# Optimization experiments

Measured on AMD Instinct MI355X. Metric: run time of the kernel, lower is better.

The kernel has to match this reference:

```python
import jax, jax.numpy as jnp
import numpy as np

N = 8192
NFEAT = 512
NHID = 512
NCLASS = 64
NLAYERS = 8
LAMDA = 0.5
ALPHA = 0.1
EDGE_P = 0.002  # ~16 avg degree


def setup_inputs() -> dict:
    key = jax.random.key(0)
    ks = jax.random.split(key, 6)
    x = jax.random.normal(ks[0], (N, NFEAT), dtype=jnp.float32)
    # sparse 0/1 adjacency, densified (the original densifies adj each layer)
    adj = (jax.random.uniform(ks[1], (N, N)) < EDGE_P).astype(jnp.float32)
    stdv1 = 1.0 / np.sqrt(NHID)
    fc1_W = jax.random.normal(ks[2], (NFEAT, NHID), dtype=jnp.float32) * stdv1
    fc1_b = jnp.zeros((NHID,), dtype=jnp.float32)
    # GraphConvolution.reset_parameters: uniform(-1/sqrt(out), 1/sqrt(out))
    conv_Ws = jax.random.uniform(ks[3], (NLAYERS, NHID, NHID), minval=-stdv1, maxval=stdv1, dtype=jnp.float32)
    stdv2 = 1.0 / np.sqrt(NCLASS)
    fc2_W = jax.random.normal(ks[4], (NHID, NCLASS), dtype=jnp.float32) * stdv2
    fc2_b = jnp.zeros((NCLASS,), dtype=jnp.float32)
    return {"x": x, "adj": adj, "fc1_W": fc1_W, "fc1_b": fc1_b,
            "conv_Ws": conv_Ws, "fc2_W": fc2_W, "fc2_b": fc2_b}


def reference(x, adj, fc1_W, fc1_b, conv_Ws, fc2_W, fc2_b):
    n = adj.shape[0]
    # A_hat = A + I ; P = D^{-1/2} A_hat D^{-1/2}  (diag matmuls -> row/col scaling)
    A_hat = adj + jnp.eye(n, dtype=adj.dtype)
    dinv = 1.0 / jnp.sqrt(jnp.sum(A_hat, axis=0))  # [N]
    P = dinv[:, None] * A_hat * dinv[None, :]      # identical every layer; compute once

    H0 = jax.nn.relu(x @ fc1_W + fc1_b)            # fc1 (dropout is identity: training=False)
    H = H0
    for i in range(NLAYERS):
        beta = float(np.log(LAMDA / (i + 1) + 1.0))
        init_res = (1.0 - ALPHA) * (P @ H) + ALPHA * H0
        # init_res @ ((1-beta) I + beta W) expanded:
        H = jax.nn.relu((1.0 - beta) * init_res + beta * (init_res @ conv_Ws[i]))
    logits = H @ fc2_W + fc2_b
    return -jax.nn.log_softmax(logits, axis=1)
```

## Files before the change

kernel.cpp:

```cpp
#include <hip/hip_runtime.h>
#include <hip/hip_bf16.h>
#include <cmath>

#define N_NODES 8192
#define NFEAT 512
#define NHID 512
#define NCLASS 64
#define NLAYERS 8
#define CAP 96

typedef __attribute__((ext_vector_type(8))) short bf16x8;
typedef __attribute__((ext_vector_type(4))) float f32x4;
typedef unsigned short u16;

__device__ inline float bf2f(short u) {
  union { unsigned int i; float f; } x;
  x.i = ((unsigned int)(u16)u) << 16;
  return x.f;
}
__device__ inline short f2bf(float f) {
  union { float f; unsigned int i; } x;
  x.f = f;
  unsigned int r = x.i + 0x7FFFu + ((x.i >> 16) & 1u);
  return (short)(r >> 16);
}

__global__ __launch_bounds__(256)
void extract_kernel(const float* __restrict__ adj, int* __restrict__ idx,
                    int* __restrict__ cnt, int* __restrict__ colcnt)
{
  __shared__ int s_cnt;
  const int i = blockIdx.x;
  if (threadIdx.x == 0) s_cnt = 0;
  __syncthreads();
  const uint4* row = (const uint4*)(adj + (size_t)i * N_NODES);
  for (int c = threadIdx.x; c < N_NODES / 4; c += 256) {
    uint4 v = row[c];
    if ((v.x | v.y | v.z | v.w) == 0u) continue;
    unsigned int vals[4] = {v.x, v.y, v.z, v.w};
    #pragma unroll
    for (int e = 0; e < 4; ++e) {
      if (vals[e] != 0u) {
        int p = atomicAdd(&s_cnt, 1);
        if (p < CAP) idx[(size_t)i * CAP + p] = c * 4 + e;
        atomicAdd(&colcnt[c * 4 + e], 1);
      }
    }
  }
  __syncthreads();
  if (threadIdx.x == 0) cnt[i] = min(s_cnt, CAP);
}

__global__ __launch_bounds__(256)
void dinv_kernel(const int* __restrict__ colcnt, float* __restrict__ dinv)
{
  int j = blockIdx.x * 256 + threadIdx.x;
  if (j < N_NODES) dinv[j] = 1.0f / sqrtf((float)colcnt[j] + 1.0f);
}

__global__ __launch_bounds__(256)
void cvt_bf16_kernel(const float* __restrict__ src, u16* __restrict__ dst, int n4)
{
  int i = blockIdx.x * 256 + threadIdx.x;
  if (i >= n4) return;
  float4 v = ((const float4*)src)[i];
  ushort4 o;
  o.x = (u16)f2bf(v.x); o.y = (u16)f2bf(v.y);
  o.z = (u16)f2bf(v.z); o.w = (u16)f2bf(v.w);
  ((ushort4*)dst)[i] = o;
}

struct Coefs { float cA[8]; float cB[8]; };

__global__ __launch_bounds__(256)
void transpose_cast_kernel(const float* __restrict__ fc1W, const float* __restrict__ convW,
                           const float* __restrict__ fc2W,
                           u16* __restrict__ Wt, u16* __restrict__ Wt2, Coefs co)
{
  __shared__ float tile[32][33];
  const int m = blockIdx.z;
  const int k0 = blockIdx.x * 32, n0 = blockIdx.y * 32;
  if (m == 9 && n0 >= 64) return;
  const int tx = threadIdx.x & 31, ty = threadIdx.x >> 5;
  if (m == 9) {
    #pragma unroll
    for (int r = 0; r < 32; r += 8)
      tile[ty + r][tx] = fc2W[(size_t)(k0 + ty + r) * 64 + n0 + tx];
    __syncthreads();
    #pragma unroll
    for (int r = 0; r < 32; r += 8)
      Wt2[(size_t)(n0 + ty + r) * 512 + k0 + tx] = (u16)f2bf(tile[tx][ty + r]);
    return;
  }
  const float* src = (m == 0) ? fc1W : convW + (size_t)(m - 1) * NHID * NHID;
  u16* dst = Wt + (size_t)m * NHID * NHID;
  float cA = 0.f, cB = 1.f;
  if (m >= 1) { cA = co.cA[m - 1]; cB = co.cB[m - 1]; }
  #pragma unroll
  for (int r = 0; r < 32; r += 8)
    tile[ty + r][tx] = src[(size_t)(k0 + ty + r) * NHID + n0 + tx];
  __syncthreads();
  #pragma unroll
  for (int r = 0; r < 32; r += 8) {
    const int krow = k0 + tx, ncol = n0 + ty + r;
    float val = cB * tile[tx][ty + r];
    if (m >= 1 && krow == ncol) val += cA;
    dst[(size_t)ncol * NHID + krow] = (u16)f2bf(val);
  }
}

#define AS1 __attribute__((address_space(1)))
#define AS3 __attribute__((address_space(3)))

__device__ inline void load16(const void* g, void* l) {
  __builtin_amdgcn_global_load_lds((const AS1 void*)g, (AS3 void*)l, 16, 0, 0);
}

template<int MODE>
__global__ __launch_bounds__(256, 4)
void gemm_kernel(const u16* __restrict__ A, const u16* __restrict__ Bt,
                 const float* __restrict__ bias, const float* __restrict__ dinv,
                 u16* __restrict__ out0, u16* __restrict__ out1,
                 float* __restrict__ outF)
{
  constexpr int K = 512;
  constexpr int N = (MODE == 3) ? NCLASS : 512;
  __shared__ u16 lds[2][2][64 * 64];
  const int tid = threadIdx.x;
  const int wave = tid >> 6, lane = tid & 63;

  const int cpx = gridDim.x >> 3;
  const int logical = (blockIdx.x & 7) * cpx + (blockIdx.x >> 3);
  const int mblk = (MODE == 3) ? logical : (logical >> 3);
  const int nblk = (MODE == 3) ? 0 : (logical & 7);
  const int m0 = mblk * 64, n0 = nblk * 64;

  const int wr = wave >> 1, wc = wave & 1;
  const int lrow = lane & 15, lk = lane >> 4;

  f32x4 acc[2][2];
  #pragma unroll
  for (int a = 0; a < 2; ++a)
    #pragma unroll
    for (int b = 0; b < 2; ++b)
      acc[a][b] = (f32x4){0.f, 0.f, 0.f, 0.f};

  auto stage = [&](int b, int ks) {
    #pragma unroll
    for (int r = 0; r < 2; ++r) {
      const int c = r * 256 + wave * 64 + lane;
      const int row = c >> 3;
      const int sc = (c & 7) ^ (row & 7);
      load16(A  + (size_t)(m0 + row) * K + ks + sc * 8, &lds[b][0][(r * 256 + wave * 64) * 8]);
      load16(Bt + (size_t)(n0 + row) * K + ks + sc * 8, &lds[b][1][(r * 256 + wave * 64) * 8]);
    }
  };

  stage(0, 0);
  __syncthreads();

  for (int t = 0; t < 8; ++t) {
    const int b = t & 1;
    if (t + 1 < 8) stage(b ^ 1, (t + 1) * 64);
    const char* pA = (const char*)lds[b][0];
    const char* pB = (const char*)lds[b][1];
    bf16x8 af[2][2], bfr[2][2];
    #pragma unroll
    for (int mi = 0; mi < 2; ++mi) {
      const int row = wr * 32 + mi * 16 + lrow;
      #pragma unroll
      for (int ks2 = 0; ks2 < 2; ++ks2) {
        const int j = ks2 * 4 + lk;
        af[mi][ks2] = *(const bf16x8*)(pA + row * 128 + ((j ^ (row & 7)) * 16));
      }
    }
    #pragma unroll
    for (int ni = 0; ni < 2; ++ni) {
      const int row = wc * 32 + ni * 16 + lrow;
      #pragma unroll
      for (int ks2 = 0; ks2 < 2; ++ks2) {
        const int j = ks2 * 4 + lk;
        bfr[ni][ks2] = *(const bf16x8*)(pB + row * 128 + ((j ^ (row & 7)) * 16));
      }
    }
    #pragma unroll
    for (int ks2 = 0; ks2 < 2; ++ks2)
      #pragma unroll
      for (int mi = 0; mi < 2; ++mi)
        #pragma unroll
        for (int ni = 0; ni < 2; ++ni)
          acc[mi][ni] = __builtin_amdgcn_mfma_f32_16x16x32_bf16(af[mi][ks2], bfr[ni][ks2], acc[mi][ni], 0, 0, 0);
    __syncthreads();
  }

  if (MODE != 3) {
    #pragma unroll
    for (int mi = 0; mi < 2; ++mi) {
      #pragma unroll
      for (int ni = 0; ni < 2; ++ni) {
        #pragma unroll
        for (int r = 0; r < 4; ++r) {
          const int row = m0 + wr * 32 + mi * 16 + lk * 4 + r;
          const int col = n0 + wc * 32 + ni * 16 + lrow;
          const size_t o = (size_t)row * N + col;
          float v = acc[mi][ni][r];
          if (MODE == 0) {
            v = fmaxf(v + bias[col], 0.f);
            out0[o] = (u16)f2bf(v);
            out1[o] = (u16)f2bf(dinv[row] * v);
          } else {
            v = fmaxf(v, 0.f);
            out0[o] = (u16)f2bf(MODE == 1 ? dinv[row] * v : v);
          }
        }
      }
    }
  } else {
    float* Cf = (float*)&lds[0][0][0];
    #pragma unroll
    for (int mi = 0; mi < 2; ++mi)
      #pragma unroll
      for (int ni = 0; ni < 2; ++ni)
        #pragma unroll
        for (int r = 0; r < 4; ++r) {
          const int row = wr * 32 + mi * 16 + lk * 4 + r;
          const int col = wc * 32 + ni * 16 + lrow;
          Cf[row * 65 + col] = acc[mi][ni][r] + bias[col];
        }
    __syncthreads();
    #pragma unroll 4
    for (int r = 0; r < 16; ++r) {
      const int row = wave * 16 + r;
      const float v = Cf[row * 65 + lane];
      float mx = v;
      #pragma unroll
      for (int off = 32; off > 0; off >>= 1) mx = fmaxf(mx, __shfl_xor(mx, off));
      float s = __expf(v - mx);
      #pragma unroll
      for (int off = 32; off > 0; off >>= 1) s += __shfl_xor(s, off);
      outF[(size_t)(m0 + row) * NCLASS + lane] = -(v - mx - logf(s));
    }
  }
}

__global__ __launch_bounds__(256)
void spmm_kernel(const u16* __restrict__ Hs, const u16* __restrict__ H0,
                 const float* __restrict__ dinv, const int* __restrict__ idx,
                 const int* __restrict__ cnt, u16* __restrict__ IR)
{
  const int wave = threadIdx.x >> 6, lane = threadIdx.x & 63;
  const int i = blockIdx.x * 4 + wave;
  const int c0 = lane * 8;
  const int n = cnt[i];
  int jreg = 0;
  if (lane < n) jreg = idx[(size_t)i * CAP + lane] & (N_NODES - 1);

  float acc[8];
  #pragma unroll
  for (int e = 0; e < 8; ++e) acc[e] = 0.f;

  const int nn = min(n, 64);
  int t = 0;
  for (; t + 8 <= nn; t += 8) {
    bf16x8 v[8];
    #pragma unroll
    for (int u = 0; u < 8; ++u) {
      const int j = __shfl(jreg, t + u);
      v[u] = *(const bf16x8*)&Hs[(size_t)j * NHID + c0];
    }
    #pragma unroll
    for (int u = 0; u < 8; ++u)
      #pragma unroll
      for (int e = 0; e < 8; ++e)
        acc[e] += bf2f(v[u][e]);
  }
  for (; t < nn; ++t) {
    const int j = __shfl(jreg, t);
    bf16x8 v = *(const bf16x8*)&Hs[(size_t)j * NHID + c0];
    #pragma unroll
    for (int e = 0; e < 8; ++e) acc[e] += bf2f(v[e]);
  }
  for (; t < n; ++t) {
    const int j = idx[(size_t)i * CAP + t] & (N_NODES - 1);
    bf16x8 v = *(const bf16x8*)&Hs[(size_t)j * NHID + c0];
    #pragma unroll
    for (int e = 0; e < 8; ++e) acc[e] += bf2f(v[e]);
  }

  const float di = dinv[i];
  bf16x8 self = *(const bf16x8*)&Hs[(size_t)i * NHID + c0];
  bf16x8 h0   = *(const bf16x8*)&H0[(size_t)i * NHID + c0];
  bf16x8 ov;
  #pragma unroll
  for (int e = 0; e < 8; ++e) {
    float v = 0.9f * di * (acc[e] + bf2f(self[e])) + 0.1f * bf2f(h0[e]);
    ov[e] = f2bf(v);
  }
  *(bf16x8*)&IR[(size_t)i * NHID + c0] = ov;
}

extern "C" void kernel_launch(void* const* d_in, const int* in_sizes, int n_in,
                              void* d_out, int out_size, void* d_ws, size_t ws_size,
                              hipStream_t stream)
{
  const float* x     = (const float*)d_in[0];
  const float* adj   = (const float*)d_in[1];
  const float* fc1W  = (const float*)d_in[2];
  const float* fc1b  = (const float*)d_in[3];
  const float* convW = (const float*)d_in[4];
  const float* fc2W  = (const float*)d_in[5];
  const float* fc2b  = (const float*)d_in[6];
  float* out = (float*)d_out;

  char* ws = (char*)d_ws;
  size_t off = 0;
  auto alloc = [&](size_t bytes) -> void* {
    void* p = ws + off;
    off = (off + bytes + 255) & ~(size_t)255;
    return p;
  };
  u16*   xb   = (u16*)alloc((size_t)N_NODES * NFEAT * 2);
  u16*   Wt   = (u16*)alloc((size_t)9 * NHID * NHID * 2);
  u16*   Wt2  = (u16*)alloc((size_t)NCLASS * NHID * 2);
  u16*   H0   = (u16*)alloc((size_t)N_NODES * NHID * 2);
  u16*   HsA  = (u16*)alloc((size_t)N_NODES * NHID * 2);
  u16*   HsB  = (u16*)alloc((size_t)N_NODES * NHID * 2);
  u16*   IR   = (u16*)alloc((size_t)N_NODES * NHID * 2);
  int*   idx  = (int*)alloc((size_t)N_NODES * CAP * 4);
  int*   cnt  = (int*)alloc((size_t)N_NODES * 4);
  int*   colc = (int*)alloc((size_t)N_NODES * 4);
  float* dinv = (float*)alloc((size_t)N_NODES * 4);

  Coefs co;
  for (int i = 0; i < NLAYERS; ++i) {
    const double beta = log(0.5 / (double)(i + 1) + 1.0);
    co.cA[i] = (float)(1.0 - beta);
    co.cB[i] = (float)beta;
  }

  hipMemsetAsync(colc, 0, N_NODES * 4, stream);
  extract_kernel<<<N_NODES, 256, 0, stream>>>(adj, idx, cnt, colc);
  dinv_kernel<<<N_NODES / 256, 256, 0, stream>>>(colc, dinv);
  cvt_bf16_kernel<<<(N_NODES * NFEAT / 4) / 256, 256, 0, stream>>>(x, xb, N_NODES * NFEAT / 4);
  transpose_cast_kernel<<<dim3(16, 16, 10), 256, 0, stream>>>(fc1W, convW, fc2W, Wt, Wt2, co);

  gemm_kernel<0><<<1024, 256, 0, stream>>>(xb, Wt, fc1b, dinv, H0, HsA, nullptr);

  const u16* Hin = HsA;
  for (int i = 0; i < NLAYERS; ++i) {
    spmm_kernel<<<N_NODES / 4, 256, 0, stream>>>(Hin, H0, dinv, idx, cnt, IR);
    u16* Hout = (Hin == HsA) ? HsB : HsA;
    if (i < NLAYERS - 1)
      gemm_kernel<1><<<1024, 256, 0, stream>>>(
          IR, Wt + (size_t)(i + 1) * NHID * NHID, nullptr, dinv, Hout, nullptr, nullptr);
    else
      gemm_kernel<2><<<1024, 256, 0, stream>>>(
          IR, Wt + (size_t)(i + 1) * NHID * NHID, nullptr, dinv, Hout, nullptr, nullptr);
    Hin = Hout;
  }

  gemm_kernel<3><<<128, 256, 0, stream>>>((const u16*)Hin, Wt2, fc2b, nullptr, nullptr, nullptr, out);
}
```

Before: 305.3 us.

## Replace LDS-tiled dense GEMMs with register-resident-B GEMM and remap SpMM blocks

Adds a new GEMM kernel for the fc1 and per-layer conv projections. Each wave keeps a 16-column slice of the transposed weight in registers and streams A rows directly from global memory, with no LDS staging or barriers. The old kernel is reduced to a dedicated fc2 plus log-softmax kernel. The SpMM block index is also remapped so consecutive blocks land on different XCD-interleaved row groups. The trade-off is more global and L2 reads of A (each row is read by 32 column blocks) and more register use, in exchange for removing sync overhead.

```diff
diff --git a/kernel.cpp b/kernel.cpp
--- a/kernel.cpp
+++ b/kernel.cpp
@@ -109,6 +109,56 @@
   }
 }
 
+template<int MODE>
+__global__ __launch_bounds__(256, 4)
+void rgemm_kernel(const u16* __restrict__ A, const u16* __restrict__ Bt,
+                  const float* __restrict__ bias, const float* __restrict__ dinv,
+                  u16* __restrict__ out0, u16* __restrict__ out1)
+{
+  constexpr int K = 512, N = 512;
+  const int wave = threadIdx.x >> 6, lane = threadIdx.x & 63;
+  const int lrow = lane & 15, lk = lane >> 4;
+  const int mw = blockIdx.x * 256 + wave * 64;
+  const int n0 = blockIdx.y * 16;
+  const int col = n0 + lrow;
+
+  bf16x8 breg[16];
+  const u16* Brow = Bt + (size_t)col * K + lk * 8;
+  #pragma unroll
+  for (int ks = 0; ks < 16; ++ks)
+    breg[ks] = *(const bf16x8*)(Brow + ks * 32);
+
+  const float bb = (MODE == 0) ? bias[col] : 0.f;
+
+  #pragma unroll
+  for (int mt = 0; mt < 4; ++mt) {
+    const u16* Arow = A + (size_t)(mw + mt * 16 + lrow) * K + lk * 8;
+    f32x4 acc0 = (f32x4){0.f, 0.f, 0.f, 0.f};
+    f32x4 acc1 = (f32x4){0.f, 0.f, 0.f, 0.f};
+    #pragma unroll
+    for (int ks = 0; ks < 16; ks += 2) {
+      bf16x8 a0 = *(const bf16x8*)(Arow + ks * 32);
+      bf16x8 a1 = *(const bf16x8*)(Arow + ks * 32 + 32);
+      acc0 = __builtin_amdgcn_mfma_f32_16x16x32_bf16(a0, breg[ks],     acc0, 0, 0, 0);
+      acc1 = __builtin_amdgcn_mfma_f32_16x16x32_bf16(a1, breg[ks + 1], acc1, 0, 0, 0);
+    }
+    #pragma unroll
+    for (int r = 0; r < 4; ++r) {
+      const int row = mw + mt * 16 + lk * 4 + r;
+      const size_t o = (size_t)row * N + col;
+      float v = acc0[r] + acc1[r];
+      if (MODE == 0) {
+        v = fmaxf(v + bb, 0.f);
+        out0[o] = (u16)f2bf(v);
+        out1[o] = (u16)f2bf(dinv[row] * v);
+      } else {
+        v = fmaxf(v, 0.f);
+        out0[o] = (u16)f2bf(MODE == 1 ? dinv[row] * v : v);
+      }
+    }
+  }
+}
+
 #define AS1 __attribute__((address_space(1)))
 #define AS3 __attribute__((address_space(3)))
 
@@ -116,25 +166,17 @@
   __builtin_amdgcn_global_load_lds((const AS1 void*)g, (AS3 void*)l, 16, 0, 0);
 }
 
-template<int MODE>
 __global__ __launch_bounds__(256, 4)
-void gemm_kernel(const u16* __restrict__ A, const u16* __restrict__ Bt,
-                 const float* __restrict__ bias, const float* __restrict__ dinv,
-                 u16* __restrict__ out0, u16* __restrict__ out1,
-                 float* __restrict__ outF)
+void fc2_kernel(const u16* __restrict__ A, const u16* __restrict__ Bt,
+                const float* __restrict__ bias, float* __restrict__ outF)
 {
   constexpr int K = 512;
-  constexpr int N = (MODE == 3) ? NCLASS : 512;
   __shared__ u16 lds[2][2][64 * 64];
   const int tid = threadIdx.x;
   const int wave = tid >> 6, lane = tid & 63;
-
   const int cpx = gridDim.x >> 3;
   const int logical = (blockIdx.x & 7) * cpx + (blockIdx.x >> 3);
-  const int mblk = (MODE == 3) ? logical : (logical >> 3);
-  const int nblk = (MODE == 3) ? 0 : (logical & 7);
-  const int m0 = mblk * 64, n0 = nblk * 64;
-
+  const int m0 = logical * 64, n0 = 0;
   const int wr = wave >> 1, wc = wave & 1;
   const int lrow = lane & 15, lk = lane >> 4;
 
@@ -193,53 +235,29 @@
     __syncthreads();
   }
 
-  if (MODE != 3) {
-    #pragma unroll
-    for (int mi = 0; mi < 2; ++mi) {
-      #pragma unroll
-      for (int ni = 0; ni < 2; ++ni) {
-        #pragma unroll
-        for (int r = 0; r < 4; ++r) {
-          const int row = m0 + wr * 32 + mi * 16 + lk * 4 + r;
-          const int col = n0 + wc * 32 + ni * 16 + lrow;
-          const size_t o = (size_t)row * N + col;
-          float v = acc[mi][ni][r];
-          if (MODE == 0) {
-            v = fmaxf(v + bias[col], 0.f);
-            out0[o] = (u16)f2bf(v);
-            out1[o] = (u16)f2bf(dinv[row] * v);
-          } else {
-            v = fmaxf(v, 0.f);
-            out0[o] = (u16)f2bf(MODE == 1 ? dinv[row] * v : v);
-          }
-        }
-      }
-    }
-  } else {
-    float* Cf = (float*)&lds[0][0][0];
-    #pragma unroll
-    for (int mi = 0; mi < 2; ++mi)
-      #pragma unroll
-      for (int ni = 0; ni < 2; ++ni)
-        #pragma unroll
-        for (int r = 0; r < 4; ++r) {
-          const int row = wr * 32 + mi * 16 + lk * 4 + r;
-          const int col = wc * 32 + ni * 16 + lrow;
-          Cf[row * 65 + col] = acc[mi][ni][r] + bias[col];
-        }
-    __syncthreads();
-    #pragma unroll 4
-    for (int r = 0; r < 16; ++r) {
-      const int row = wave * 16 + r;
-      const float v = Cf[row * 65 + lane];
-      float mx = v;
-      #pragma unroll
-      for (int off = 32; off > 0; off >>= 1) mx = fmaxf(mx, __shfl_xor(mx, off));
-      float s = __expf(v - mx);
-      #pragma unroll
-      for (int off = 32; off > 0; off >>= 1) s += __shfl_xor(s, off);
-      outF[(size_t)(m0 + row) * NCLASS + lane] = -(v - mx - logf(s));
-    }
+  float* Cf = (float*)&lds[0][0][0];
+  #pragma unroll
+  for (int mi = 0; mi < 2; ++mi)
+    #pragma unroll
+    for (int ni = 0; ni < 2; ++ni)
+      #pragma unroll
+      for (int r = 0; r < 4; ++r) {
+        const int row = wr * 32 + mi * 16 + lk * 4 + r;
+        const int cc = wc * 32 + ni * 16 + lrow;
+        if (cc < NCLASS) Cf[row * 65 + cc] = acc[mi][ni][r] + bias[cc];
+      }
+  __syncthreads();
+  #pragma unroll 4
+  for (int r = 0; r < 16; ++r) {
+    const int row = wave * 16 + r;
+    const float v = Cf[row * 65 + lane];
+    float mx = v;
+    #pragma unroll
+    for (int off = 32; off > 0; off >>= 1) mx = fmaxf(mx, __shfl_xor(mx, off));
+    float s = __expf(v - mx);
+    #pragma unroll
+    for (int off = 32; off > 0; off >>= 1) s += __shfl_xor(s, off);
+    outF[(size_t)(m0 + row) * NCLASS + lane] = -(v - mx - logf(s));
   }
 }
 
@@ -249,7 +267,10 @@
                  const int* __restrict__ cnt, u16* __restrict__ IR)
 {
   const int wave = threadIdx.x >> 6, lane = threadIdx.x & 63;
-  const int i = blockIdx.x * 4 + wave;
+  const int b = blockIdx.x;
+  const int c = (b & 7) + 8 * ((b >> 3) >> 6);
+  const int j64 = (b >> 3) & 63;
+  const int i = (c * 64 + j64) * 4 + wave;
   const int c0 = lane * 8;
   const int n = cnt[i];
   int jreg = 0;
@@ -344,20 +365,20 @@
   cvt_bf16_kernel<<<(N_NODES * NFEAT / 4) / 256, 256, 0, stream>>>(x, xb, N_NODES * NFEAT / 4);
   transpose_cast_kernel<<<dim3(16, 16, 10), 256, 0, stream>>>(fc1W, convW, fc2W, Wt, Wt2, co);
 
-  gemm_kernel<0><<<1024, 256, 0, stream>>>(xb, Wt, fc1b, dinv, H0, HsA, nullptr);
+  rgemm_kernel<0><<<dim3(32, 32), 256, 0, stream>>>(xb, Wt, fc1b, dinv, H0, HsA);
 
   const u16* Hin = HsA;
   for (int i = 0; i < NLAYERS; ++i) {
     spmm_kernel<<<N_NODES / 4, 256, 0, stream>>>(Hin, H0, dinv, idx, cnt, IR);
     u16* Hout = (Hin == HsA) ? HsB : HsA;
     if (i < NLAYERS - 1)
-      gemm_kernel<1><<<1024, 256, 0, stream>>>(
-          IR, Wt + (size_t)(i + 1) * NHID * NHID, nullptr, dinv, Hout, nullptr, nullptr);
+      rgemm_kernel<1><<<dim3(32, 32), 256, 0, stream>>>(
+          IR, Wt + (size_t)(i + 1) * NHID * NHID, nullptr, dinv, Hout, nullptr);
     else
-      gemm_kernel<2><<<1024, 256, 0, stream>>>(
-          IR, Wt + (size_t)(i + 1) * NHID * NHID, nullptr, dinv, Hout, nullptr, nullptr);
+      rgemm_kernel<2><<<dim3(32, 32), 256, 0, stream>>>(
+          IR, Wt + (size_t)(i + 1) * NHID * NHID, nullptr, dinv, Hout, nullptr);
     Hin = Hout;
   }
 
-  gemm_kernel<3><<<128, 256, 0, stream>>>((const u16*)Hin, Wt2, fc2b, nullptr, nullptr, nullptr, out);
-}
+  fc2_kernel<<<128, 256, 0, stream>>>((const u16*)Hin, Wt2, fc2b, out);
+}
```

New measurement: 568.0 us. 1.86x slower.

## Merge preprocessing kernels, triple-buffer GEMM loads, compute dinv inline

Applied to the files above, without the earlier changes.

Extraction, input bf16 cast and weight transpose/cast now run as one front kernel with block-range dispatch, and the separate dinv kernel is dropped in favour of computing rsqrt(colcnt+1) inline where it is used. The GEMM goes from double to triple LDS buffering, with manual vmcnt waits plus a barrier so loads run two stages ahead, and its occupancy hint is lowered to 3. This cuts kernel launches and deepens load/compute overlap, at the cost of more LDS per block and possibly lower occupancy.

```diff
diff --git a/kernel.cpp b/kernel.cpp
--- a/kernel.cpp
+++ b/kernel.cpp
@@ -13,6 +13,8 @@
 typedef __attribute__((ext_vector_type(4))) float f32x4;
 typedef unsigned short u16;
 
+struct Coefs { float cA[8]; float cB[8]; };
+
 __device__ inline float bf2f(short u) {
   union { unsigned int i; float f; } x;
   x.i = ((unsigned int)(u16)u) << 16;
@@ -26,60 +28,59 @@
 }
 
 __global__ __launch_bounds__(256)
-void extract_kernel(const float* __restrict__ adj, int* __restrict__ idx,
-                    int* __restrict__ cnt, int* __restrict__ colcnt)
+void front_kernel(const float* __restrict__ adj, int* __restrict__ idx,
+                  int* __restrict__ cnt, int* __restrict__ colcnt,
+                  const float* __restrict__ x, u16* __restrict__ xb,
+                  const float* __restrict__ fc1W, const float* __restrict__ convW,
+                  const float* __restrict__ fc2W,
+                  u16* __restrict__ Wt, u16* __restrict__ Wt2, Coefs co)
 {
-  __shared__ int s_cnt;
-  const int i = blockIdx.x;
-  if (threadIdx.x == 0) s_cnt = 0;
-  __syncthreads();
-  const uint4* row = (const uint4*)(adj + (size_t)i * N_NODES);
-  for (int c = threadIdx.x; c < N_NODES / 4; c += 256) {
-    uint4 v = row[c];
-    if ((v.x | v.y | v.z | v.w) == 0u) continue;
-    unsigned int vals[4] = {v.x, v.y, v.z, v.w};
-    #pragma unroll
-    for (int e = 0; e < 4; ++e) {
-      if (vals[e] != 0u) {
-        int p = atomicAdd(&s_cnt, 1);
-        if (p < CAP) idx[(size_t)i * CAP + p] = c * 4 + e;
-        atomicAdd(&colcnt[c * 4 + e], 1);
+  __shared__ char smraw[4224];
+  const int bid = blockIdx.x;
+
+  if (bid < 8192) {
+    int* s_cnt = (int*)smraw;
+    const int i = bid;
+    if (threadIdx.x == 0) *s_cnt = 0;
+    __syncthreads();
+    const uint4* row = (const uint4*)(adj + (size_t)i * N_NODES);
+    for (int c = threadIdx.x; c < N_NODES / 4; c += 256) {
+      uint4 v = row[c];
+      if ((v.x | v.y | v.z | v.w) == 0u) continue;
+      unsigned int vals[4] = {v.x, v.y, v.z, v.w};
+      #pragma unroll
+      for (int e = 0; e < 4; ++e) {
+        if (vals[e] != 0u) {
+          int p = atomicAdd(s_cnt, 1);
+          if (p < CAP) idx[(size_t)i * CAP + p] = c * 4 + e;
+          atomicAdd(&colcnt[c * 4 + e], 1);
+        }
       }
     }
-  }
-  __syncthreads();
-  if (threadIdx.x == 0) cnt[i] = min(s_cnt, CAP);
-}
-
-__global__ __launch_bounds__(256)
-void dinv_kernel(const int* __restrict__ colcnt, float* __restrict__ dinv)
-{
-  int j = blockIdx.x * 256 + threadIdx.x;
-  if (j < N_NODES) dinv[j] = 1.0f / sqrtf((float)colcnt[j] + 1.0f);
-}
-
-__global__ __launch_bounds__(256)
-void cvt_bf16_kernel(const float* __restrict__ src, u16* __restrict__ dst, int n4)
-{
-  int i = blockIdx.x * 256 + threadIdx.x;
-  if (i >= n4) return;
-  float4 v = ((const float4*)src)[i];
-  ushort4 o;
-  o.x = (u16)f2bf(v.x); o.y = (u16)f2bf(v.y);
-  o.z = (u16)f2bf(v.z); o.w = (u16)f2bf(v.w);
-  ((ushort4*)dst)[i] = o;
-}
-
-struct Coefs { float cA[8]; float cB[8]; };
-
-__global__ __launch_bounds__(256)
-void transpose_cast_kernel(const float* __restrict__ fc1W, const float* __restrict__ convW,
-                           const float* __restrict__ fc2W,
-                           u16* __restrict__ Wt, u16* __restrict__ Wt2, Coefs co)
-{
-  __shared__ float tile[32][33];
-  const int m = blockIdx.z;
-  const int k0 = blockIdx.x * 32, n0 = blockIdx.y * 32;
+    __syncthreads();
+    if (threadIdx.x == 0) cnt[i] = min(*s_cnt, CAP);
+    return;
+  }
+
+  if (bid < 9216) {
+    const int base = (bid - 8192) * 256 + threadIdx.x;
+    const float4* src = (const float4*)x;
+    #pragma unroll
+    for (int it = 0; it < 4; ++it) {
+      const int i = it * (1024 * 256) + base;
+      float4 v = src[i];
+      ushort4 o;
+      o.x = (u16)f2bf(v.x); o.y = (u16)f2bf(v.y);
+      o.z = (u16)f2bf(v.z); o.w = (u16)f2bf(v.w);
+      ((ushort4*)xb)[i] = o;
+    }
+    return;
+  }
+
+  float (*tile)[33] = (float(*)[33])smraw;
+  const int vb = bid - 9216;
+  const int m = vb >> 8;
+  const int k0 = (vb & 15) * 32, n0 = ((vb >> 4) & 15) * 32;
   if (m == 9 && n0 >= 64) return;
   const int tx = threadIdx.x & 31, ty = threadIdx.x >> 5;
   if (m == 9) {
@@ -117,15 +118,15 @@
 }
 
 template<int MODE>
-__global__ __launch_bounds__(256, 4)
+__global__ __launch_bounds__(256, 3)
 void gemm_kernel(const u16* __restrict__ A, const u16* __restrict__ Bt,
-                 const float* __restrict__ bias, const float* __restrict__ dinv,
+                 const float* __restrict__ bias, const int* __restrict__ colc,
                  u16* __restrict__ out0, u16* __restrict__ out1,
                  float* __restrict__ outF)
 {
   constexpr int K = 512;
   constexpr int N = (MODE == 3) ? NCLASS : 512;
-  __shared__ u16 lds[2][2][64 * 64];
+  __shared__ u16 lds[3][2][64 * 64];
   const int tid = threadIdx.x;
   const int wave = tid >> 6, lane = tid & 63;
 
@@ -157,11 +158,13 @@
   };
 
   stage(0, 0);
-  __syncthreads();
+  stage(1, 64);
 
   for (int t = 0; t < 8; ++t) {
-    const int b = t & 1;
-    if (t + 1 < 8) stage(b ^ 1, (t + 1) * 64);
+    if (t < 7) asm volatile("s_waitcnt vmcnt(4)\n\ts_barrier" ::: "memory");
+    else       asm volatile("s_waitcnt vmcnt(0)\n\ts_barrier" ::: "memory");
+    if (t + 2 < 8) stage((t + 2) % 3, (t + 2) * 64);
+    const int b = t % 3;
     const char* pA = (const char*)lds[b][0];
     const char* pB = (const char*)lds[b][1];
     bf16x8 af[2][2], bfr[2][2];
@@ -190,7 +193,6 @@
         #pragma unroll
         for (int ni = 0; ni < 2; ++ni)
           acc[mi][ni] = __builtin_amdgcn_mfma_f32_16x16x32_bf16(af[mi][ks2], bfr[ni][ks2], acc[mi][ni], 0, 0, 0);
-    __syncthreads();
   }
 
   if (MODE != 3) {
@@ -206,16 +208,22 @@
           float v = acc[mi][ni][r];
           if (MODE == 0) {
             v = fmaxf(v + bias[col], 0.f);
+            const float di = rsqrtf((float)colc[row] + 1.0f);
             out0[o] = (u16)f2bf(v);
-            out1[o] = (u16)f2bf(dinv[row] * v);
+            out1[o] = (u16)f2bf(di * v);
+          } else if (MODE == 1) {
+            v = fmaxf(v, 0.f);
+            const float di = rsqrtf((float)colc[row] + 1.0f);
+            out0[o] = (u16)f2bf(di * v);
           } else {
             v = fmaxf(v, 0.f);
-            out0[o] = (u16)f2bf(MODE == 1 ? dinv[row] * v : v);
+            out0[o] = (u16)f2bf(v);
           }
         }
       }
     }
   } else {
+    __syncthreads();
     float* Cf = (float*)&lds[0][0][0];
     #pragma unroll
     for (int mi = 0; mi < 2; ++mi)
@@ -224,8 +232,8 @@
         #pragma unroll
         for (int r = 0; r < 4; ++r) {
           const int row = wr * 32 + mi * 16 + lk * 4 + r;
-          const int col = wc * 32 + ni * 16 + lrow;
-          Cf[row * 65 + col] = acc[mi][ni][r] + bias[col];
+          const int cc = wc * 32 + ni * 16 + lrow;
+          if (cc < NCLASS) Cf[row * 65 + cc] = acc[mi][ni][r] + bias[cc];
         }
     __syncthreads();
     #pragma unroll 4
@@ -245,7 +253,7 @@
 
 __global__ __launch_bounds__(256)
 void spmm_kernel(const u16* __restrict__ Hs, const u16* __restrict__ H0,
-                 const float* __restrict__ dinv, const int* __restrict__ idx,
+                 const int* __restrict__ colc, const int* __restrict__ idx,
                  const int* __restrict__ cnt, u16* __restrict__ IR)
 {
   const int wave = threadIdx.x >> 6, lane = threadIdx.x & 63;
@@ -287,7 +295,7 @@
     for (int e = 0; e < 8; ++e) acc[e] += bf2f(v[e]);
   }
 
-  const float di = dinv[i];
+  const float di = rsqrtf((float)colc[i] + 1.0f);
   bf16x8 self = *(const bf16x8*)&Hs[(size_t)i * NHID + c0];
   bf16x8 h0   = *(const bf16x8*)&H0[(size_t)i * NHID + c0];
   bf16x8 ov;
@@ -329,7 +337,6 @@
   int*   idx  = (int*)alloc((size_t)N_NODES * CAP * 4);
   int*   cnt  = (int*)alloc((size_t)N_NODES * 4);
   int*   colc = (int*)alloc((size_t)N_NODES * 4);
-  float* dinv = (float*)alloc((size_t)N_NODES * 4);
 
   Coefs co;
   for (int i = 0; i < NLAYERS; ++i) {
@@ -338,24 +345,22 @@
     co.cB[i] = (float)beta;
   }
 
-  hipMemsetAsync(colc, 0, N_NODES * 4, stream);
-  extract_kernel<<<N_NODES, 256, 0, stream>>>(adj, idx, cnt, colc);
-  dinv_kernel<<<N_NODES / 256, 256, 0, stream>>>(colc, dinv);
-  cvt_bf16_kernel<<<(N_NODES * NFEAT / 4) / 256, 256, 0, stream>>>(x, xb, N_NODES * NFEAT / 4);
-  transpose_cast_kernel<<<dim3(16, 16, 10), 256, 0, stream>>>(fc1W, convW, fc2W, Wt, Wt2, co);
-
-  gemm_kernel<0><<<1024, 256, 0, stream>>>(xb, Wt, fc1b, dinv, H0, HsA, nullptr);
+  hipMemsetAsync(colc, 0, (size_t)N_NODES * 4, stream);
+  front_kernel<<<8192 + 1024 + 2560, 256, 0, stream>>>(
+      adj, idx, cnt, colc, x, xb, fc1W, convW, fc2W, Wt, Wt2, co);
+
+  gemm_kernel<0><<<1024, 256, 0, stream>>>(xb, Wt, fc1b, colc, H0, HsA, nullptr);
 
   const u16* Hin = HsA;
   for (int i = 0; i < NLAYERS; ++i) {
-    spmm_kernel<<<N_NODES / 4, 256, 0, stream>>>(Hin, H0, dinv, idx, cnt, IR);
+    spmm_kernel<<<N_NODES / 4, 256, 0, stream>>>(Hin, H0, colc, idx, cnt, IR);
     u16* Hout = (Hin == HsA) ? HsB : HsA;
     if (i < NLAYERS - 1)
       gemm_kernel<1><<<1024, 256, 0, stream>>>(
-          IR, Wt + (size_t)(i + 1) * NHID * NHID, nullptr, dinv, Hout, nullptr, nullptr);
+          IR, Wt + (size_t)(i + 1) * NHID * NHID, nullptr, colc, Hout, nullptr, nullptr);
     else
       gemm_kernel<2><<<1024, 256, 0, stream>>>(
-          IR, Wt + (size_t)(i + 1) * NHID * NHID, nullptr, dinv, Hout, nullptr, nullptr);
+          IR, Wt + (size_t)(i + 1) * NHID * NHID, nullptr, colc, Hout, nullptr, nullptr);
     Hin = Hout;
   }
 
```

Measured after the change: 308.2 us. About the same (+1.0%).
